# Optimization experiments

Hardware: AMD Instinct MI355X
Metric: run time of the kernel (lower is better)

The kernel has to match this reference:

```python
import jax, jax.numpy as jnp
import numpy as np

ALPHA = 0.2  # LeakyReLU negative slope


def _head(x, W, b, a, eye):
    # x: [B,N,F], W: [F,D], a: [2D,1], eye: [N,N] identity
    h = x @ W + b                                   # [B,N,D]
    D = W.shape[1]
    # additive attention: score[i,j] = leakyrelu(a_l . h_i + a_r . h_j)
    s = jax.nn.leaky_relu(h @ a[:D] + jnp.swapaxes(h @ a[D:], 1, 2), ALPHA)  # [B,N,N]
    s = jnp.where(eye > 0, -jnp.inf, s)             # mask diagonal (adj_identity)
    p = jax.nn.softmax(s, axis=-1) + eye            # softmax then add identity
    return jax.nn.elu(p @ h)                        # [B,N,D]


def setup_inputs() -> dict:
    key = jax.random.key(0)
    ks = jax.random.split(key, 16)
    B, N, F_IN, HID, HEADS = 8, 2048, 256, 256, 2
    D = HID // HEADS
    inp = {
        "x": jax.random.normal(ks[0], (B, N, F_IN), dtype=jnp.float32),
        "edges": jax.random.randint(ks[1], (B, N), 0, N, dtype=jnp.int64),
    }
    i = 2
    for layer in range(2):
        fin = F_IN if layer == 0 else HID
        for head in range(HEADS):
            inp[f"W_{layer}_{head}"] = jax.random.normal(ks[i], (fin, D), dtype=jnp.float32) * (1.0 / np.sqrt(fin)); i += 1
            inp[f"b_{layer}_{head}"] = jnp.zeros((D,), dtype=jnp.float32)
            inp[f"a_{layer}_{head}"] = jax.random.normal(ks[i], (2 * D, 1), dtype=jnp.float32) * 0.1; i += 1
    return inp


def reference(x, edges, W_0_0, b_0_0, a_0_0, W_0_1, b_0_1, a_0_1,
              W_1_0, b_1_0, a_1_0, W_1_1, b_1_1, a_1_1):
    N = x.shape[1]
    eye = jnp.eye(N, dtype=x.dtype)
    layers = [
        [(W_0_0, b_0_0, a_0_0), (W_0_1, b_0_1, a_0_1)],
        [(W_1_0, b_1_0, a_1_0), (W_1_1, b_1_1, a_1_1)],
    ]
    for heads in layers:
        x = jnp.concatenate([_head(x, W, b, a, eye) for (W, b, a) in heads], axis=-1)
    return x
```

## Files before the change

### kernel.cpp

```cpp
#include <hip/hip_runtime.h>
#include <math.h>

#define ALPHA_SLOPE 0.2f

typedef _Float16 f16;
typedef f16 f16x4 __attribute__((ext_vector_type(4)));
typedef f16 f16x8 __attribute__((ext_vector_type(8)));
typedef float f32x4 __attribute__((ext_vector_type(4)));

constexpr int B_ = 8, N = 2048, D = 128, H = 2;
constexpr int C2 = H * D;
constexpr int M_ = B_ * N;
constexpr int NCH = 32;
constexpr int CHL = N / NCH;

__device__ __forceinline__ float lrelu(float x) { return fmaxf(x, ALPHA_SLOPE * x); }

__global__ __launch_bounds__(256) void cvtW_kernel(
    const float* __restrict__ W00, const float* __restrict__ W01,
    const float* __restrict__ W10, const float* __restrict__ W11,
    f16* __restrict__ WcT)
{
    const int t = threadIdx.x;
    const int w = blockIdx.x;
#pragma unroll
    for (int p = 0; p < 4; ++p) {
        const int pair = w * 4 + p;
        const int layer = pair >> 8, c = pair & 255;
        const float* __restrict__ W0 = layer ? W10 : W00;
        const float* __restrict__ W1 = layer ? W11 : W01;
        const float v = (c < D) ? W0[t * D + c] : W1[t * D + (c - D)];
        WcT[(size_t)layer * C2 * C2 + c * C2 + t] = (f16)v;
    }
}

__global__ __launch_bounds__(256) void gemm_lr_kernel(
    const float* __restrict__ x32, const f16* __restrict__ xh,
    const f16* __restrict__ Wl,
    const float* __restrict__ b0, const float* __restrict__ b1,
    const float* __restrict__ a0, const float* __restrict__ a1,
    f16* __restrict__ h,
    float* __restrict__ l0, float* __restrict__ r0,
    float* __restrict__ l1, float* __restrict__ r1,
    const int use32)
{
    __shared__ f16 hts[32][C2 + 8];
    const int t = threadIdx.x;
    const int row0 = blockIdx.x * 32;
    if (use32) {
#pragma unroll
        for (int p = 0; p < 8; ++p) {
            const int q = p * 256 + t;
            const int row = q >> 6, c4 = q & 63;
            const float4 v = *(const float4*)&x32[(size_t)(row0 + row) * C2 + c4 * 4];
            f16x4 o; o[0] = (f16)v.x; o[1] = (f16)v.y; o[2] = (f16)v.z; o[3] = (f16)v.w;
            *(f16x4*)&hts[row][c4 * 4] = o;
        }
    } else {
#pragma unroll
        for (int p = 0; p < 4; ++p) {
            const int q = p * 256 + t;
            const int row = q >> 5, cc = q & 31;
            *(f16x8*)&hts[row][cc * 8] = *(const f16x8*)&xh[(size_t)(row0 + row) * C2 + cc * 8];
        }
    }
    __syncthreads();
    const int w = t >> 6, l = t & 63;
    const int fm = l & 15, fk = (l >> 4) * 8;
    f32x4 acc[2][4] = {};
#pragma unroll
    for (int ks = 0; ks < 8; ++ks) {
        f16x8 af[2], bf[4];
#pragma unroll
        for (int rt = 0; rt < 2; ++rt)
            af[rt] = *(const f16x8*)&hts[rt * 16 + fm][ks * 32 + fk];
#pragma unroll
        for (int ct = 0; ct < 4; ++ct) {
            const int col = w * 64 + ct * 16 + fm;
            bf[ct] = *(const f16x8*)&Wl[(size_t)col * C2 + ks * 32 + fk];
        }
#pragma unroll
        for (int rt = 0; rt < 2; ++rt)
#pragma unroll
            for (int ct = 0; ct < 4; ++ct)
                acc[rt][ct] = __builtin_amdgcn_mfma_f32_16x16x32_f16(af[rt], bf[ct], acc[rt][ct], 0, 0, 0);
    }
    __syncthreads();
#pragma unroll
    for (int rt = 0; rt < 2; ++rt)
#pragma unroll
        for (int ct = 0; ct < 4; ++ct) {
            const int col = w * 64 + ct * 16 + fm;
            const float bias = (col < D) ? b0[col] : b1[col - D];
#pragma unroll
            for (int q = 0; q < 4; ++q) {
                const int row = rt * 16 + (l >> 4) * 4 + q;
                hts[row][col] = (f16)(acc[rt][ct][q] + bias);
            }
        }
    __syncthreads();
#pragma unroll
    for (int p = 0; p < 4; ++p) {
        const int q = p * 256 + t;
        const int row = q >> 5, cc = q & 31;
        *(f16x8*)&h[(size_t)(row0 + row) * C2 + cc * 8] = *(const f16x8*)&hts[row][cc * 8];
    }
    const int lrow = t >> 3;
    const int oct = t & 7;
    const float* __restrict__ ab = (oct >= 4) ? a1 : a0;
    float lv = 0.f, rv = 0.f;
#pragma unroll
    for (int c4 = 0; c4 < 8; ++c4) {
        const int cc = (c4 + oct) & 7;
        const int col = oct * 32 + cc * 4;
        const int cih = (oct & 3) * 32 + cc * 4;
        const f16x4 hf = *(const f16x4*)&hts[lrow][col];
        const float4 alv = *(const float4*)&ab[cih];
        const float4 arv = *(const float4*)&ab[128 + cih];
        const float h0 = (float)hf[0], h1 = (float)hf[1], h2 = (float)hf[2], h3 = (float)hf[3];
        lv += h0 * alv.x + h1 * alv.y + h2 * alv.z + h3 * alv.w;
        rv += h0 * arv.x + h1 * arv.y + h2 * arv.z + h3 * arv.w;
    }
    lv += __shfl_xor(lv, 1, 64); lv += __shfl_xor(lv, 2, 64);
    rv += __shfl_xor(rv, 1, 64); rv += __shfl_xor(rv, 2, 64);
    const int grow = row0 + lrow;
    if (oct == 0) { l0[grow] = lv; r0[grow] = rv; }
    else if (oct == 4) { l1[grow] = lv; r1[grow] = rv; }
}

__global__ __launch_bounds__(1024) void rank_kernel(
    const float* __restrict__ r0, const float* __restrict__ r1,
    const float* __restrict__ l0, const float* __restrict__ l1,
    float* __restrict__ rs_s, int* __restrict__ perm, int* __restrict__ kout)
{
    const int bh = blockIdx.y;
    const float* __restrict__ r = ((bh & 1) ? r1 : r0) + (size_t)(bh >> 1) * N;
    const float* __restrict__ lp = ((bh & 1) ? l1 : l0) + (size_t)(bh >> 1) * N;
    __shared__ float rl[N];
    __shared__ int scnt[16][64], sk2[16][64];
    const int t = threadIdx.x;
    for (int j = t; j < N; j += 1024) rl[j] = r[j];
    __syncthreads();
    const int el = t & 63;
    const int q = t >> 6;
    const int e = blockIdx.x * 64 + el;
    const float re = rl[e];
    const float thr = -lp[e];
    const int qm = blockIdx.x >> 1;
    int cnt = 0, k2 = 0;
    const int jlo = q * 128, jhi = jlo + 128;
    if (q < qm) {
        for (int j = jlo; j < jhi; j += 4) {
            const float4 v = *(const float4*)&rl[j];
            cnt += (v.x >= re) + (v.y >= re) + (v.z >= re) + (v.w >= re);
            k2  += (v.x >= thr) + (v.y >= thr) + (v.z >= thr) + (v.w >= thr);
        }
    } else if (q > qm) {
        for (int j = jlo; j < jhi; j += 4) {
            const float4 v = *(const float4*)&rl[j];
            cnt += (v.x > re) + (v.y > re) + (v.z > re) + (v.w > re);
            k2  += (v.x >= thr) + (v.y >= thr) + (v.z >= thr) + (v.w >= thr);
        }
    } else {
        for (int j = jlo; j < jhi; j += 4) {
            const float4 v = *(const float4*)&rl[j];
            cnt += (v.x > re) || (v.x == re && (j + 0) < e);
            cnt += (v.y > re) || (v.y == re && (j + 1) < e);
            cnt += (v.z > re) || (v.z == re && (j + 2) < e);
            cnt += (v.w > re) || (v.w == re && (j + 3) < e);
            k2  += (v.x >= thr) + (v.y >= thr) + (v.z >= thr) + (v.w >= thr);
        }
    }
    scnt[q][el] = cnt; sk2[q][el] = k2;
    __syncthreads();
    if (t < 64) {
        int c = 0, kk = 0;
#pragma unroll
        for (int qq = 0; qq < 16; ++qq) { c += scnt[qq][t]; kk += sk2[qq][t]; }
        const int eg = blockIdx.x * 64 + t;
        const size_t g = (size_t)bh * N;
        rs_s[g + c] = rl[eg];
        perm[g + c] = eg;
        kout[g + eg] = kk;
    }
}

__global__ __launch_bounds__(256) void scanA_kernel(
    const f16* __restrict__ h, const int* __restrict__ perm,
    const float* __restrict__ rs_s,
    f16* __restrict__ PA, f16* __restrict__ PB,
    float* __restrict__ SAloc, float* __restrict__ SBloc,
    float* __restrict__ totA, float* __restrict__ totB,
    float* __restrict__ stA, float* __restrict__ stB)
{
    __shared__ f16 hs[CHL][D];
    __shared__ int pj[CHL];
    __shared__ float wA[CHL], wB[CHL];
    __shared__ float buf[2 * CHL];
    const int chunk = blockIdx.x, bh = blockIdx.y;
    const int b = bh >> 1, head = bh & 1;
    const int t = threadIdx.x;
    const size_t g = (size_t)bh * N + chunk * CHL;
    const float c1 = rs_s[(size_t)bh * N];
    if (t < CHL) {
        pj[t] = perm[g + t];
        const float rr = rs_s[g + t];
        const float eA = __expf(rr - c1);
        const float eB = __expf(0.2f * (rr - c1));
        wA[t] = eA; wB[t] = eB;
        buf[t] = eA;
    } else if (t < 2 * CHL) {
        const float rr = rs_s[g + (CHL - 1 - (t - CHL))];
        buf[t] = __expf(0.2f * (rr - c1));
    }
    __syncthreads();
    const int li = t & (CHL - 1);
#pragma unroll
    for (int off = 1; off < CHL; off <<= 1) {
        const float v = (t < 2 * CHL && li >= off) ? buf[t - off] : 0.f;
        __syncthreads();
        if (t < 2 * CHL && li >= off) buf[t] += v;
        __syncthreads();
    }
    if (t < CHL) SAloc[g + t] = buf[t];
    else if (t < 2 * CHL) SBloc[g + (CHL - 1 - li)] = buf[t];
    if (t == CHL - 1) stA[bh * NCH + chunk] = buf[CHL - 1];
    if (t == 2 * CHL - 1) stB[bh * NCH + chunk] = buf[2 * CHL - 1];
#pragma unroll
    for (int p = 0; p < 4; ++p) {
        const int q = p * 256 + t;
        const int row = q >> 4, c8 = q & 15;
        const f16* src = h + (size_t)(b * N + pj[row]) * C2 + head * D;
        *(f16x8*)&hs[row][c8 * 8] = *(const f16x8*)&src[c8 * 8];
    }
    __syncthreads();
    if (t < D) {
        const int d = t;
        float acc = 0.f;
        for (int j = 0; j < CHL; ++j) {
            acc = fmaf(wA[j], (float)hs[j][d], acc);
            PA[(g + j) * D + d] = (f16)acc;
        }
        totA[(size_t)(bh * NCH + chunk) * D + d] = acc;
    } else {
        const int d = t - D;
        float acc = 0.f;
        for (int jj = 0; jj < CHL; ++jj) {
            const int j = CHL - 1 - jj;
            acc = fmaf(wB[j], (float)hs[j][d], acc);
            PB[(g + j) * D + d] = (f16)acc;
        }
        totB[(size_t)(bh * NCH + chunk) * D + d] = acc;
    }
}

__global__ __launch_bounds__(256) void scanOff_kernel(
    const float* __restrict__ totA, const float* __restrict__ totB,
    const float* __restrict__ stA, const float* __restrict__ stB,
    float* __restrict__ AOff, float* __restrict__ BOffS,
    float* __restrict__ lsAg, float* __restrict__ lsBg)
{
    const int bh = blockIdx.x;
    const int t = threadIdx.x;
    const size_t base = (size_t)bh * NCH;
    if (t < D) {
        const int d = t;
        float acc = 0.f;
#pragma unroll
        for (int ch = 0; ch < NCH; ++ch) {
            const float tmp = totA[(base + ch) * D + d];
            AOff[(base + ch) * D + d] = acc;
            acc += tmp;
        }
    } else {
        const int d = t - D;
        float acc = 0.f;
#pragma unroll
        for (int ch = NCH - 1; ch >= 0; --ch) {
            const float tmp = totB[(base + ch) * D + d];
            BOffS[(base + ch) * D + d] = acc;
            acc += tmp;
        }
    }
    if (t == 0) {
        float a = 0.f;
#pragma unroll
        for (int q = 0; q < NCH; ++q) { const float tmp = stA[base + q]; lsAg[base + q] = a; a += tmp; }
    } else if (t == 64) {
        float a = 0.f;
#pragma unroll
        for (int q = NCH - 1; q >= 0; --q) { const float tmp = stB[base + q]; lsBg[base + q] = a; a += tmp; }
    }
}

__global__ __launch_bounds__(256) void out_kernel(
    const f16* __restrict__ h,
    const float* __restrict__ l0v, const float* __restrict__ l1v,
    const float* __restrict__ r0v, const float* __restrict__ r1v,
    const int* __restrict__ perm, const float* __restrict__ rs_s,
    const int* __restrict__ kout,
    const float* __restrict__ SAloc, const float* __restrict__ SBloc,
    const float* __restrict__ lsAg, const float* __restrict__ lsBg,
    const float* __restrict__ AOff, const float* __restrict__ BOffS,
    const f16* __restrict__ PA, const f16* __restrict__ PB,
    float* __restrict__ out_f32, f16* __restrict__ out_f16, const int final_layer)
{
    const int head = blockIdx.y, b = blockIdx.z;
    const int bh = b * H + head;
    const float* __restrict__ lv = (head ? l1v : l0v) + (size_t)b * N;
    const float* __restrict__ rv = (head ? r1v : r0v) + (size_t)b * N;
    const int t = threadIdx.x;
    const size_t gb = (size_t)bh * N;
    const size_t obase = (size_t)bh * NCH;

    const int i = blockIdx.x * 16 + (t >> 4);
    const int c0 = (t & 15) * 8;
    const float li = lv[i];
    const float ri = rv[i];
    const float rmx1 = rs_s[gb];
    const float rmx2 = rs_s[gb + 1];
    const int rdx = perm[gb];
    const float rmx = (i == rdx) ? rmx2 : rmx1;
    const float m = lrelu(li + rmx);
    const float alpha = __expf(li + rmx1 - m);
    const float beta = __expf(0.2f * (li + rmx1) - m);
    const float diag = __expf(lrelu(li + ri) - m);

    const int k = kout[gb + i];
    const float SAk = (k > 0) ? (lsAg[obase + ((k - 1) >> 6)] + SAloc[gb + k - 1]) : 0.f;
    const float SBk = (k < N) ? (lsBg[obase + (k >> 6)] + SBloc[gb + k]) : 0.f;
    const float Z = fmaf(alpha, SAk, beta * SBk) - diag;
    const float invZ = 1.f / Z;

    float pa[8] = {}, pb[8] = {};
    if (k > 0) {
        const int kk = k - 1, ch = kk >> 6;
        const f16x8 v = *(const f16x8*)&PA[(gb + kk) * D + c0];
        const float4 o0 = *(const float4*)&AOff[(obase + ch) * D + c0];
        const float4 o1 = *(const float4*)&AOff[(obase + ch) * D + c0 + 4];
        pa[0] = (float)v[0] + o0.x; pa[1] = (float)v[1] + o0.y;
        pa[2] = (float)v[2] + o0.z; pa[3] = (float)v[3] + o0.w;
        pa[4] = (float)v[4] + o1.x; pa[5] = (float)v[5] + o1.y;
        pa[6] = (float)v[6] + o1.z; pa[7] = (float)v[7] + o1.w;
    }
    if (k < N) {
        const int ch = k >> 6;
        const f16x8 v = *(const f16x8*)&PB[(gb + k) * D + c0];
        const float4 o0 = *(const float4*)&BOffS[(obase + ch) * D + c0];
        const float4 o1 = *(const float4*)&BOffS[(obase + ch) * D + c0 + 4];
        pb[0] = (float)v[0] + o0.x; pb[1] = (float)v[1] + o0.y;
        pb[2] = (float)v[2] + o0.z; pb[3] = (float)v[3] + o0.w;
        pb[4] = (float)v[4] + o1.x; pb[5] = (float)v[5] + o1.y;
        pb[6] = (float)v[6] + o1.z; pb[7] = (float)v[7] + o1.w;
    }

    const f16x8 hraw = *(const f16x8*)&h[(size_t)(b * N + i) * C2 + head * D + c0];
    float o[8];
#pragma unroll
    for (int q = 0; q < 8; ++q) {
        const float hv = (float)hraw[q];
        const float num = alpha * pa[q] + beta * pb[q] - diag * hv;
        float v = fmaf(num, invZ, hv);
        o[q] = v > 0.f ? v : (__expf(v) - 1.f);
    }
    const size_t oidx = (size_t)(b * N + i) * C2 + head * D + c0;
    if (final_layer) {
        *(float4*)&out_f32[oidx] = make_float4(o[0], o[1], o[2], o[3]);
        *(float4*)&out_f32[oidx + 4] = make_float4(o[4], o[5], o[6], o[7]);
    } else {
        f16x8 ov;
#pragma unroll
        for (int q = 0; q < 8; ++q) ov[q] = (f16)o[q];
        *(f16x8*)&out_f16[oidx] = ov;
    }
}

extern "C" void kernel_launch(void* const* d_in, const int* in_sizes, int n_in,
                              void* d_out, int out_size, void* d_ws, size_t ws_size,
                              hipStream_t stream)
{
    float* ws = (float*)d_ws;
    size_t off = 0;
    f16* xh = (f16*)(ws + off);   off += (size_t)M_ * C2 / 2;
    f16* WcT = (f16*)(ws + off);  off += (size_t)C2 * C2;
    f16* h = (f16*)(ws + off);    off += (size_t)M_ * C2 / 2;
    float* l0 = ws + off;         off += (size_t)B_ * N;
    float* r0 = ws + off;         off += (size_t)B_ * N;
    float* l1 = ws + off;         off += (size_t)B_ * N;
    float* r1 = ws + off;         off += (size_t)B_ * N;
    float* rs_s = ws + off;       off += (size_t)16 * N;
    int* perm = (int*)(ws + off); off += (size_t)16 * N;
    int* kout = (int*)(ws + off); off += (size_t)16 * N;
    float* SAloc = ws + off;      off += (size_t)16 * N;
    float* SBloc = ws + off;      off += (size_t)16 * N;
    f16* PA = (f16*)(ws + off);   off += (size_t)16 * N * D / 2;
    f16* PB = (f16*)(ws + off);   off += (size_t)16 * N * D / 2;
    float* totA = ws + off;       off += (size_t)16 * NCH * D;
    float* totB = ws + off;       off += (size_t)16 * NCH * D;
    float* stA = ws + off;        off += (size_t)16 * NCH;
    float* stB = ws + off;        off += (size_t)16 * NCH;
    float* AOff = ws + off;       off += (size_t)16 * NCH * D;
    float* BOffS = ws + off;      off += (size_t)16 * NCH * D;
    float* lsAg = ws + off;       off += (size_t)16 * NCH;
    float* lsBg = ws + off;       off += (size_t)16 * NCH;

    const float* x32 = (const float*)d_in[0];

    cvtW_kernel<<<128, 256, 0, stream>>>(
        (const float*)d_in[2], (const float*)d_in[5],
        (const float*)d_in[8], (const float*)d_in[11], WcT);

    for (int layer = 0; layer < 2; ++layer) {
        const int base = 2 + layer * 6;
        const float* b0 = (const float*)d_in[base + 1];
        const float* a0 = (const float*)d_in[base + 2];
        const float* b1 = (const float*)d_in[base + 4];
        const float* a1 = (const float*)d_in[base + 5];

        gemm_lr_kernel<<<M_ / 32, 256, 0, stream>>>(
            x32, xh, WcT + (size_t)layer * C2 * C2, b0, b1, a0, a1,
            h, l0, r0, l1, r1, layer == 0 ? 1 : 0);
        rank_kernel<<<dim3(N / 64, B_ * H), 1024, 0, stream>>>(
            r0, r1, l0, l1, rs_s, perm, kout);
        scanA_kernel<<<dim3(NCH, B_ * H), 256, 0, stream>>>(
            h, perm, rs_s, PA, PB, SAloc, SBloc, totA, totB, stA, stB);
        scanOff_kernel<<<B_ * H, 256, 0, stream>>>(
            totA, totB, stA, stB, AOff, BOffS, lsAg, lsBg);
        out_kernel<<<dim3(N / 16, H, B_), 256, 0, stream>>>(
            h, l0, l1, r0, r1, perm, rs_s, kout, SAloc, SBloc, lsAg, lsBg,
            AOff, BOffS, PA, PB, (float*)d_out, xh, layer == 1 ? 1 : 0);
    }
}
```

Measured before the change: 182.1 us.

## Widen gemm and scan kernels to 1024 threads with split sequential scan

The gemm_lr kernel now runs 16 waves per block, each computing one 16-column tile, instead of 4 waves computing four tiles each. The scanA kernel splits the 64-step sequential prefix scan into four 16-step segments handled by separate thread groups, then combines segment offsets through shared memory. Both changes aim to expose more parallelism and cut the serial dependency chain and latency per block. In exchange there are larger blocks, extra synchronisation, more register use for the buffered values, and redundant A-tile loads across waves.

```diff
diff --git a/kernel.cpp b/kernel.cpp
--- a/kernel.cpp
+++ b/kernel.cpp
@@ -34,7 +34,7 @@
     }
 }
 
-__global__ __launch_bounds__(256) void gemm_lr_kernel(
+__global__ __launch_bounds__(1024) void gemm_lr_kernel(
     const float* __restrict__ x32, const f16* __restrict__ xh,
     const f16* __restrict__ Wl,
     const float* __restrict__ b0, const float* __restrict__ b1,
@@ -49,83 +49,74 @@
     const int row0 = blockIdx.x * 32;
     if (use32) {
 #pragma unroll
-        for (int p = 0; p < 8; ++p) {
-            const int q = p * 256 + t;
+        for (int p = 0; p < 2; ++p) {
+            const int q = p * 1024 + t;
             const int row = q >> 6, c4 = q & 63;
             const float4 v = *(const float4*)&x32[(size_t)(row0 + row) * C2 + c4 * 4];
             f16x4 o; o[0] = (f16)v.x; o[1] = (f16)v.y; o[2] = (f16)v.z; o[3] = (f16)v.w;
             *(f16x4*)&hts[row][c4 * 4] = o;
         }
     } else {
-#pragma unroll
-        for (int p = 0; p < 4; ++p) {
-            const int q = p * 256 + t;
-            const int row = q >> 5, cc = q & 31;
-            *(f16x8*)&hts[row][cc * 8] = *(const f16x8*)&xh[(size_t)(row0 + row) * C2 + cc * 8];
-        }
+        const int q = t;
+        const int row = q >> 5, cc = q & 31;
+        *(f16x8*)&hts[row][cc * 8] = *(const f16x8*)&xh[(size_t)(row0 + row) * C2 + cc * 8];
     }
     __syncthreads();
     const int w = t >> 6, l = t & 63;
     const int fm = l & 15, fk = (l >> 4) * 8;
-    f32x4 acc[2][4] = {};
+    const int col = w * 16 + fm;
+    f32x4 acc[2] = {};
 #pragma unroll
     for (int ks = 0; ks < 8; ++ks) {
-        f16x8 af[2], bf[4];
+        f16x8 af[2], bf;
 #pragma unroll
         for (int rt = 0; rt < 2; ++rt)
             af[rt] = *(const f16x8*)&hts[rt * 16 + fm][ks * 32 + fk];
-#pragma unroll
-        for (int ct = 0; ct < 4; ++ct) {
-            const int col = w * 64 + ct * 16 + fm;
-            bf[ct] = *(const f16x8*)&Wl[(size_t)col * C2 + ks * 32 + fk];
-        }
+        bf = *(const f16x8*)&Wl[(size_t)col * C2 + ks * 32 + fk];
 #pragma unroll
         for (int rt = 0; rt < 2; ++rt)
-#pragma unroll
-            for (int ct = 0; ct < 4; ++ct)
-                acc[rt][ct] = __builtin_amdgcn_mfma_f32_16x16x32_f16(af[rt], bf[ct], acc[rt][ct], 0, 0, 0);
-    }
-    __syncthreads();
-#pragma unroll
-    for (int rt = 0; rt < 2; ++rt)
-#pragma unroll
-        for (int ct = 0; ct < 4; ++ct) {
-            const int col = w * 64 + ct * 16 + fm;
-            const float bias = (col < D) ? b0[col] : b1[col - D];
+            acc[rt] = __builtin_amdgcn_mfma_f32_16x16x32_f16(af[rt], bf, acc[rt], 0, 0, 0);
+    }
+    __syncthreads();
+    {
+        const float bias = (col < D) ? b0[col] : b1[col - D];
+#pragma unroll
+        for (int rt = 0; rt < 2; ++rt)
 #pragma unroll
             for (int q = 0; q < 4; ++q) {
                 const int row = rt * 16 + (l >> 4) * 4 + q;
-                hts[row][col] = (f16)(acc[rt][ct][q] + bias);
+                hts[row][col] = (f16)(acc[rt][q] + bias);
             }
-        }
-    __syncthreads();
-#pragma unroll
-    for (int p = 0; p < 4; ++p) {
-        const int q = p * 256 + t;
+    }
+    __syncthreads();
+    {
+        const int q = t;
         const int row = q >> 5, cc = q & 31;
         *(f16x8*)&h[(size_t)(row0 + row) * C2 + cc * 8] = *(const f16x8*)&hts[row][cc * 8];
     }
-    const int lrow = t >> 3;
-    const int oct = t & 7;
-    const float* __restrict__ ab = (oct >= 4) ? a1 : a0;
-    float lv = 0.f, rv = 0.f;
-#pragma unroll
-    for (int c4 = 0; c4 < 8; ++c4) {
-        const int cc = (c4 + oct) & 7;
-        const int col = oct * 32 + cc * 4;
-        const int cih = (oct & 3) * 32 + cc * 4;
-        const f16x4 hf = *(const f16x4*)&hts[lrow][col];
-        const float4 alv = *(const float4*)&ab[cih];
-        const float4 arv = *(const float4*)&ab[128 + cih];
-        const float h0 = (float)hf[0], h1 = (float)hf[1], h2 = (float)hf[2], h3 = (float)hf[3];
-        lv += h0 * alv.x + h1 * alv.y + h2 * alv.z + h3 * alv.w;
-        rv += h0 * arv.x + h1 * arv.y + h2 * arv.z + h3 * arv.w;
-    }
-    lv += __shfl_xor(lv, 1, 64); lv += __shfl_xor(lv, 2, 64);
-    rv += __shfl_xor(rv, 1, 64); rv += __shfl_xor(rv, 2, 64);
-    const int grow = row0 + lrow;
-    if (oct == 0) { l0[grow] = lv; r0[grow] = rv; }
-    else if (oct == 4) { l1[grow] = lv; r1[grow] = rv; }
+    if (t < 256) {
+        const int lrow = t >> 3;
+        const int oct = t & 7;
+        const float* __restrict__ ab = (oct >= 4) ? a1 : a0;
+        float lv = 0.f, rv = 0.f;
+#pragma unroll
+        for (int c4 = 0; c4 < 8; ++c4) {
+            const int cc = (c4 + oct) & 7;
+            const int colx = oct * 32 + cc * 4;
+            const int cih = (oct & 3) * 32 + cc * 4;
+            const f16x4 hf = *(const f16x4*)&hts[lrow][colx];
+            const float4 alv = *(const float4*)&ab[cih];
+            const float4 arv = *(const float4*)&ab[128 + cih];
+            const float h0 = (float)hf[0], h1 = (float)hf[1], h2 = (float)hf[2], h3 = (float)hf[3];
+            lv += h0 * alv.x + h1 * alv.y + h2 * alv.z + h3 * alv.w;
+            rv += h0 * arv.x + h1 * arv.y + h2 * arv.z + h3 * arv.w;
+        }
+        lv += __shfl_xor(lv, 1, 64); lv += __shfl_xor(lv, 2, 64);
+        rv += __shfl_xor(rv, 1, 64); rv += __shfl_xor(rv, 2, 64);
+        const int grow = row0 + lrow;
+        if (oct == 0) { l0[grow] = lv; r0[grow] = rv; }
+        else if (oct == 4) { l1[grow] = lv; r1[grow] = rv; }
+    }
 }
 
 __global__ __launch_bounds__(1024) void rank_kernel(
@@ -185,7 +176,7 @@
     }
 }
 
-__global__ __launch_bounds__(256) void scanA_kernel(
+__global__ __launch_bounds__(1024) void scanA_kernel(
     const f16* __restrict__ h, const int* __restrict__ perm,
     const float* __restrict__ rs_s,
     f16* __restrict__ PA, f16* __restrict__ PB,
@@ -197,6 +188,7 @@
     __shared__ int pj[CHL];
     __shared__ float wA[CHL], wB[CHL];
     __shared__ float buf[2 * CHL];
+    __shared__ float subA[4][D], subB[4][D];
     const int chunk = blockIdx.x, bh = blockIdx.y;
     const int b = bh >> 1, head = bh & 1;
     const int t = threadIdx.x;
@@ -226,31 +218,54 @@
     else if (t < 2 * CHL) SBloc[g + (CHL - 1 - li)] = buf[t];
     if (t == CHL - 1) stA[bh * NCH + chunk] = buf[CHL - 1];
     if (t == 2 * CHL - 1) stB[bh * NCH + chunk] = buf[2 * CHL - 1];
-#pragma unroll
-    for (int p = 0; p < 4; ++p) {
-        const int q = p * 256 + t;
-        const int row = q >> 4, c8 = q & 15;
+    {
+        const int row = t >> 4, c8 = t & 15;
         const f16* src = h + (size_t)(b * N + pj[row]) * C2 + head * D;
         *(f16x8*)&hs[row][c8 * 8] = *(const f16x8*)&src[c8 * 8];
     }
     __syncthreads();
-    if (t < D) {
-        const int d = t;
+    const int s = t >> 8;
+    const int u = t & 255;
+    const int jbase = s * 16;
+    float vals[16];
+    if (u < D) {
+        const int d = u;
         float acc = 0.f;
-        for (int j = 0; j < CHL; ++j) {
-            acc = fmaf(wA[j], (float)hs[j][d], acc);
-            PA[(g + j) * D + d] = (f16)acc;
-        }
-        totA[(size_t)(bh * NCH + chunk) * D + d] = acc;
-    } else {
-        const int d = t - D;
+#pragma unroll
+        for (int jj = 0; jj < 16; ++jj) {
+            acc = fmaf(wA[jbase + jj], (float)hs[jbase + jj][d], acc);
+            vals[jj] = acc;
+        }
+        subA[s][d] = acc;
+    } else {
+        const int d = u - D;
         float acc = 0.f;
-        for (int jj = 0; jj < CHL; ++jj) {
-            const int j = CHL - 1 - jj;
-            acc = fmaf(wB[j], (float)hs[j][d], acc);
-            PB[(g + j) * D + d] = (f16)acc;
-        }
-        totB[(size_t)(bh * NCH + chunk) * D + d] = acc;
+#pragma unroll
+        for (int jj = 15; jj >= 0; --jj) {
+            acc = fmaf(wB[jbase + jj], (float)hs[jbase + jj][d], acc);
+            vals[jj] = acc;
+        }
+        subB[s][d] = acc;
+    }
+    __syncthreads();
+    if (u < D) {
+        const int d = u;
+        float offA = 0.f;
+#pragma unroll
+        for (int ss = 0; ss < 3; ++ss) if (ss < s) offA += subA[ss][d];
+#pragma unroll
+        for (int jj = 0; jj < 16; ++jj)
+            PA[(g + jbase + jj) * D + d] = (f16)(vals[jj] + offA);
+        if (s == 3) totA[(size_t)(bh * NCH + chunk) * D + d] = offA + subA[3][d];
+    } else {
+        const int d = u - D;
+        float offB = 0.f;
+#pragma unroll
+        for (int ss = 1; ss < 4; ++ss) if (ss > s) offB += subB[ss][d];
+#pragma unroll
+        for (int jj = 0; jj < 16; ++jj)
+            PB[(g + jbase + jj) * D + d] = (f16)(vals[jj] + offB);
+        if (s == 0) totB[(size_t)(bh * NCH + chunk) * D + d] = offB + subB[0][d];
     }
 }
 
@@ -417,12 +432,12 @@
         const float* b1 = (const float*)d_in[base + 4];
         const float* a1 = (const float*)d_in[base + 5];
 
-        gemm_lr_kernel<<<M_ / 32, 256, 0, stream>>>(
+        gemm_lr_kernel<<<M_ / 32, 1024, 0, stream>>>(
             x32, xh, WcT + (size_t)layer * C2 * C2, b0, b1, a0, a1,
             h, l0, r0, l1, r1, layer == 0 ? 1 : 0);
         rank_kernel<<<dim3(N / 64, B_ * H), 1024, 0, stream>>>(
             r0, r1, l0, l1, rs_s, perm, kout);
-        scanA_kernel<<<dim3(NCH, B_ * H), 256, 0, stream>>>(
+        scanA_kernel<<<dim3(NCH, B_ * H), 1024, 0, stream>>>(
             h, perm, rs_s, PA, PB, SAloc, SBloc, totA, totB, stA, stB);
         scanOff_kernel<<<B_ * H, 256, 0, stream>>>(
             totA, totB, stA, stB, AOff, BOffS, lsAg, lsBg);
```

Measured after the change: 181.4 us. About the same (-0.4%).
